# Optimization experiments

Hardware: AMD Instinct MI355X
Metric: run time of the kernel (lower is better)

## Reference

```python
import jax, jax.numpy as jnp
import numpy as np

N = 2048   # nodes in the input graph
NB = 2048  # nodes in the barycenter graph
D = 128    # embedding (feature) dimension
K = 16     # number of atoms (len(size_atoms))


def cost_mat(cost_s, cost_t, p_s, p_t, tran, emb_s, emb_t):
    """Fused Gromov-Wasserstein cost matrix.

    GW structural part:  (C_s^2 p_s) 1^T + 1 (p_t^T (C_t^2)^T) - 2 C_s T C_t^T
    Fused feature part:  0.5 * squared Euclidean distance between node embeddings.
    """
    f1 = (cost_s ** 2) @ p_s                     # (N, 1)
    f2 = p_t.T @ (cost_t ** 2).T                 # (1, NB)
    cost = f1 + f2 - 2.0 * (cost_s @ tran) @ cost_t.T  # (N, NB)
    # pairwise squared Euclidean distances between embeddings
    d_emb = (jnp.sum(emb_s ** 2, axis=1, keepdims=True)
             + jnp.sum(emb_t ** 2, axis=1)[None, :]
             - 2.0 * emb_s @ emb_t.T)            # (N, NB)
    return cost + 0.5 * d_emb


def setup_inputs() -> dict:
    key = jax.random.key(0)
    k = jax.random.split(key, 6)
    graph = jax.random.uniform(k[0], (N, N), dtype=jnp.float32)
    embedding = jax.random.normal(k[1], (N, D), dtype=jnp.float32)
    prob = jnp.ones((N, 1), jnp.float32) / N           # uniform node distribution
    graph_b = jax.random.uniform(k[2], (NB, NB), dtype=jnp.float32)
    embedding_b = jax.random.normal(k[3], (NB, D), dtype=jnp.float32)
    prob_b = jnp.ones((NB, 1), jnp.float32) / NB
    t = jax.random.uniform(k[4], (N, NB), dtype=jnp.float32)
    tran = t / jnp.sum(t)                              # valid coupling-like plan (sums to 1)
    weights = jax.nn.softmax(jax.random.normal(k[5], (K,), dtype=jnp.float32))
    return {"graph": graph, "embedding": embedding, "prob": prob,
            "graph_b": graph_b, "embedding_b": embedding_b, "prob_b": prob_b,
            "tran": tran, "weights": weights, "ole_coeff": 1, "idx": 0}


def reference(graph, embedding, prob, graph_b, embedding_b, prob_b, tran, weights, ole_coeff, idx):
    # NOTE: the torch forward also computes cluster/entropy (OLE) losses from
    # `weights`, but they do NOT enter the returned value, which is only
    # <cost_mat(...), tran>. We therefore return exactly that inner product.
    cost = cost_mat(graph, graph_b, prob, prob_b, tran, embedding, embedding_b)
    return jnp.sum(cost * tran)
```

## Files before the change

### kernel.cpp

```cpp
#include <hip/hip_runtime.h>
#include <hip/hip_bf16.h>

#define NN 2048
#define DD 128

typedef unsigned short u16;
typedef unsigned int u32;
typedef __attribute__((ext_vector_type(8))) short bf16x8;
typedef __attribute__((ext_vector_type(4))) float f32x4;

__device__ __forceinline__ u16 f2bf(float f){
  u32 u = __float_as_uint(f);
  u32 r = (u + 0x7fffu + ((u >> 16) & 1u)) >> 16;
  return (u16)r;
}

__device__ __forceinline__ void gload16(const void* g, void* l){
  __builtin_amdgcn_global_load_lds(
      (const __attribute__((address_space(1))) u32*)g,
      (__attribute__((address_space(3))) u32*)l, 16, 0, 0);
}


__device__ __forceinline__ void rowpass_graph_body(
    int bid, int tid, const float* __restrict__ src, const float* __restrict__ w,
    u16* __restrict__ dst, float* __restrict__ red){
  int wid = tid >> 6, lane = tid & 63;
  int row = bid * 4 + wid;
  const float4* s4 = (const float4*)(src + (size_t)row * NN);
  float acc = 0.f;
  #pragma unroll
  for (int it = 0; it < NN / 256; ++it){
    int c4 = it * 64 + lane;
    float4 v = s4[c4];
    float4 ww = ((const float4*)w)[c4];
    acc += v.x*v.x*ww.x + v.y*v.y*ww.y + v.z*v.z*ww.z + v.w*v.w*ww.w;
    ushort4 o; o.x = f2bf(v.x); o.y = f2bf(v.y); o.z = f2bf(v.z); o.w = f2bf(v.w);
    ((ushort4*)(dst + (size_t)row * NN))[c4] = o;
  }
  #pragma unroll
  for (int off = 32; off; off >>= 1) acc += __shfl_down(acc, off);
  if (lane == 0) red[row] = acc;
}

__device__ __forceinline__ void tran_pass_body(
    int bx, int by, int t, float (*tile)[65],
    const float* __restrict__ src,
    u16* __restrict__ Tm, u16* __restrict__ Tt,
    float* __restrict__ rs, float* __restrict__ cls)
{
  int r0 = bx * 64, c0 = by * 64;
  #pragma unroll
  for (int it = 0; it < 4; ++it){
    int chunk = it * 256 + t; int r = chunk >> 4, c4 = chunk & 15;
    float4 v = ((const float4*)(src + (size_t)(r0 + r) * NN + c0))[c4];
    tile[r][c4*4+0] = v.x; tile[r][c4*4+1] = v.y;
    tile[r][c4*4+2] = v.z; tile[r][c4*4+3] = v.w;
    ushort4 o; o.x = f2bf(v.x); o.y = f2bf(v.y); o.z = f2bf(v.z); o.w = f2bf(v.w);
    ((ushort4*)(Tm + (size_t)(r0 + r) * NN + c0))[c4] = o;
  }
  __syncthreads();
  #pragma unroll
  for (int it = 0; it < 4; ++it){
    int chunk = it * 256 + t; int j = chunk >> 4, i4 = chunk & 15;
    ushort4 o;
    o.x = f2bf(tile[i4*4+0][j]); o.y = f2bf(tile[i4*4+1][j]);
    o.z = f2bf(tile[i4*4+2][j]); o.w = f2bf(tile[i4*4+3][j]);
    ((ushort4*)(Tt + (size_t)(c0 + j) * NN + r0))[i4] = o;
  }
  {
    int r = t >> 2, cq = (t & 3) * 16;
    float s = 0.f;
    #pragma unroll
    for (int c = 0; c < 16; ++c) s += tile[r][cq + c];
    s += __shfl_down(s, 2);
    s += __shfl_down(s, 1);
    if ((t & 3) == 0) atomicAdd(&rs[r0 + r], s);
  }
  {
    int c = t >> 2, rq = (t & 3) * 16;
    float s = 0.f;
    #pragma unroll
    for (int r = 0; r < 16; ++r) s += tile[rq + r][c];
    s += __shfl_down(s, 2);
    s += __shfl_down(s, 1);
    if ((t & 3) == 0) atomicAdd(&cls[c0 + c], s);
  }
}

__device__ __forceinline__ void graphb_pass_body(
    int bx, int by, int t, float (*tile)[65], float* pb,
    const float* __restrict__ src, const float* __restrict__ probb,
    u16* __restrict__ CtT, float* __restrict__ f2)
{
  int r0 = bx * 64, c0 = by * 64;
  if (t < 64) pb[t] = probb[c0 + t];
  #pragma unroll
  for (int it = 0; it < 4; ++it){
    int chunk = it * 256 + t; int r = chunk >> 4, c4 = chunk & 15;
    float4 v = ((const float4*)(src + (size_t)(r0 + r) * NN + c0))[c4];
    tile[r][c4*4+0] = v.x; tile[r][c4*4+1] = v.y;
    tile[r][c4*4+2] = v.z; tile[r][c4*4+3] = v.w;
  }
  __syncthreads();
  #pragma unroll
  for (int it = 0; it < 4; ++it){
    int chunk = it * 256 + t; int j = chunk >> 4, i4 = chunk & 15;
    ushort4 o;
    o.x = f2bf(tile[i4*4+0][j]); o.y = f2bf(tile[i4*4+1][j]);
    o.z = f2bf(tile[i4*4+2][j]); o.w = f2bf(tile[i4*4+3][j]);
    ((ushort4*)(CtT + (size_t)(c0 + j) * NN + r0))[i4] = o;
  }
  {
    int r = t >> 2, cq = (t & 3) * 16;
    float s = 0.f;
    #pragma unroll
    for (int c = 0; c < 16; ++c){ float v = tile[r][cq + c]; s += v * v * pb[cq + c]; }
    s += __shfl_down(s, 2);
    s += __shfl_down(s, 1);
    if ((t & 3) == 0) atomicAdd(&f2[r0 + r], s);
  }
}

__device__ __forceinline__ void emb_body(
    int bid, int t, const float* __restrict__ src, u16* __restrict__ dst,
    float* __restrict__ nrm){
  int rloc = t >> 5, lane32 = t & 31;
  int row = bid * 8 + rloc;
  float4 v = ((const float4*)(src + (size_t)row * DD))[lane32];
  float a = v.x*v.x + v.y*v.y + v.z*v.z + v.w*v.w;
  ushort4 o; o.x = f2bf(v.x); o.y = f2bf(v.y); o.z = f2bf(v.z); o.w = f2bf(v.w);
  ((ushort4*)(dst + (size_t)row * DD))[lane32] = o;
  #pragma unroll
  for (int off = 16; off; off >>= 1) a += __shfl_down(a, off, 32);
  if (lane32 == 0) nrm[row] = a;
}

__global__ __launch_bounds__(256) void k_prep(
    const float* __restrict__ graph,  const float* __restrict__ prob,
    const float* __restrict__ tran,   const float* __restrict__ graphb,
    const float* __restrict__ probb,  const float* __restrict__ emb,
    const float* __restrict__ embb,
    u16* Cs, u16* Tm, u16* Tt, u16* CtT, u16* es, u16* et,
    float* f1, float* f2, float* rs, float* cls, float* ss, float* st)
{
  __shared__ float tile[64][65];
  __shared__ float pb[64];
  int b = blockIdx.x, t = threadIdx.x;
  if (b < 512){
    rowpass_graph_body(b, t, graph, prob, Cs, f1);
  } else if (b < 1536){
    int b2 = b - 512;  tran_pass_body(b2 & 31, b2 >> 5, t, tile, tran, Tm, Tt, rs, cls);
  } else if (b < 2560){
    int b2 = b - 1536; graphb_pass_body(b2 & 31, b2 >> 5, t, tile, pb, graphb, probb, CtT, f2);
  } else if (b < 2816){
    emb_body(b - 2560, t, emb, es, ss);
  } else {
    emb_body(b - 2816, t, embb, et, st);
  }
}

__global__ __launch_bounds__(512, 2) void k_gw(
    const u16* __restrict__ Cs, const u16* __restrict__ Tt,
    const u16* __restrict__ Tm, const u16* __restrict__ CtT,
    float* __restrict__ accs)
{
  __shared__ u16 lds[2][4][8192];
  const int tid = threadIdx.x;
  const int bid = blockIdx.x;
  const int swz = (bid & 7) * 32 + (bid >> 3);
  const int bi = swz >> 4, bk = swz & 15;

  const u16* srcs[4] = {Cs, Tt, Tm, CtT};
  const int panels[4] = {bi * 128, bk * 128, bi * 128, bk * 128};

  const int w = tid >> 6, lane = tid & 63;
  const int l15 = lane & 15, g = lane >> 4;
  const int gsel = w >> 2, wg = w & 3, wr = wg >> 1, wc = wg & 1;

  const int s_row = tid >> 3;
  const int s_gslot = (tid & 7) ^ (s_row & 7);

  f32x4 acc[4][4];
  #pragma unroll
  for (int m = 0; m < 4; ++m)
    #pragma unroll
    for (int n = 0; n < 4; ++n)
      acc[m][n] = (f32x4){0.f, 0.f, 0.f, 0.f};

  int offA[4][2], offB[4][2];
  #pragma unroll
  for (int m = 0; m < 4; ++m){
    int row = wr * 64 + m * 16 + l15;
    int rowb = wc * 64 + m * 16 + l15;
    #pragma unroll
    for (int kk = 0; kk < 2; ++kk){
      offA[m][kk] = row * 64 + ((((kk << 2) | g)) ^ (row & 7)) * 8;
      offB[m][kk] = rowb * 64 + ((((kk << 2) | g)) ^ (rowb & 7)) * 8;
    }
  }

  auto stage = [&](int buf, int kt){
    const size_t col = (size_t)kt * 64 + s_gslot * 8;
    #pragma unroll
    for (int tt = 0; tt < 4; ++tt){
      gload16(srcs[tt] + (size_t)(panels[tt] + s_row) * NN + col,
              &lds[buf][tt][w * 512]);
      gload16(srcs[tt] + (size_t)(panels[tt] + s_row + 64) * NN + col,
              &lds[buf][tt][4096 + w * 512]);
    }
  };

  const int NT = NN / 64;
  stage(0, 0);
  stage(1, 1);
  for (int kt = 0; kt < NT; ++kt){
    int cur = kt & 1;
    asm volatile("s_waitcnt vmcnt(8)" ::: "memory");
    __builtin_amdgcn_s_barrier();

    const u16* tA = &lds[cur][gsel * 2][0];
    const u16* tB = &lds[cur][gsel * 2 + 1][0];
    bf16x8 av[4][2], bv[4][2];
    #pragma unroll
    for (int kk = 0; kk < 2; ++kk){
      #pragma unroll
      for (int m = 0; m < 4; ++m) av[m][kk] = *(const bf16x8*)(tA + offA[m][kk]);
      #pragma unroll
      for (int n = 0; n < 4; ++n) bv[n][kk] = *(const bf16x8*)(tB + offB[n][kk]);
    }
    #pragma unroll
    for (int kk = 0; kk < 2; ++kk)
      #pragma unroll
      for (int m = 0; m < 4; ++m)
        #pragma unroll
        for (int n = 0; n < 4; ++n)
          acc[m][n] = __builtin_amdgcn_mfma_f32_16x16x32_bf16(av[m][kk], bv[n][kk], acc[m][n], 0, 0, 0);

    __builtin_amdgcn_s_barrier();

    int kn = (kt + 2 < NT) ? (kt + 2) : (NT - 1);
    stage(cur, kn);
  }

  __syncthreads();

  float* ustash = (float*)&lds[0][0][0];
  if (gsel == 0){
    #pragma unroll
    for (int m = 0; m < 4; ++m)
      #pragma unroll
      for (int n = 0; n < 4; ++n)
        #pragma unroll
        for (int r = 0; r < 4; ++r){
          int row = wr * 64 + m * 16 + g * 4 + r;
          int col = wc * 64 + n * 16 + l15;
          ustash[row * 128 + col] = acc[m][n][r];
        }
  }
  __syncthreads();
  if (gsel == 1){
    float part = 0.f;
    #pragma unroll
    for (int m = 0; m < 4; ++m)
      #pragma unroll
      for (int n = 0; n < 4; ++n)
        #pragma unroll
        for (int r = 0; r < 4; ++r){
          int row = wr * 64 + m * 16 + g * 4 + r;
          int col = wc * 64 + n * 16 + l15;
          part += acc[m][n][r] * ustash[row * 128 + col];
        }
    #pragma unroll
    for (int off = 32; off; off >>= 1) part += __shfl_down(part, off);
    if (lane == 0) atomicAdd(&accs[0], part);
  }
}

__global__ __launch_bounds__(256, 2) void k_embdot(
    const u16* __restrict__ es, const u16* __restrict__ et,
    const float* __restrict__ tran, float* __restrict__ accs)
{
  __shared__ u16 lds[2][16384];
  const int tid = threadIdx.x;
  const int bid = blockIdx.x;
  const int swz = (bid & 7) * 32 + (bid >> 3);
  const int bi = swz >> 4, bj = swz & 15;
  const int w = tid >> 6, lane = tid & 63;
  const int l15 = lane & 15, g = lane >> 4;
  const int wr = w >> 1, wc = w & 1;

  const u16* srcs[2] = {es, et};
  const int panels[2] = {bi * 128, bj * 128};

  #pragma unroll
  for (int tt = 0; tt < 2; ++tt){
    #pragma unroll
    for (int it = 0; it < 8; ++it){
      int chunk = w * 8 + it;
      int r = chunk * 4 + g;
      int s = l15 ^ (r & 15);
      gload16(srcs[tt] + (size_t)(panels[tt] + r) * DD + s * 8,
              &lds[tt][chunk * 512]);
    }
  }
  __syncthreads();

  f32x4 acc[4][4];
  #pragma unroll
  for (int m = 0; m < 4; ++m)
    #pragma unroll
    for (int n = 0; n < 4; ++n)
      acc[m][n] = (f32x4){0.f, 0.f, 0.f, 0.f};

  #pragma unroll
  for (int ks = 0; ks < 4; ++ks){
    bf16x8 av[4], bv[4];
    #pragma unroll
    for (int m = 0; m < 4; ++m){
      int row = wr * 64 + m * 16 + l15;
      int sp = (ks * 4 + g) ^ (row & 15);
      av[m] = *(const bf16x8*)((const char*)&lds[0][0] + row * 256 + sp * 16);
    }
    #pragma unroll
    for (int n = 0; n < 4; ++n){
      int rowb = wc * 64 + n * 16 + l15;
      int spb = (ks * 4 + g) ^ (rowb & 15);
      bv[n] = *(const bf16x8*)((const char*)&lds[1][0] + rowb * 256 + spb * 16);
    }
    #pragma unroll
    for (int m = 0; m < 4; ++m)
      #pragma unroll
      for (int n = 0; n < 4; ++n)
        acc[m][n] = __builtin_amdgcn_mfma_f32_16x16x32_bf16(av[m], bv[n], acc[m][n], 0, 0, 0);
  }

  float part = 0.f;
  #pragma unroll
  for (int m = 0; m < 4; ++m)
    #pragma unroll
    for (int n = 0; n < 4; ++n)
      #pragma unroll
      for (int r = 0; r < 4; ++r){
        int row = bi * 128 + wr * 64 + m * 16 + g * 4 + r;
        int col = bj * 128 + wc * 64 + n * 16 + l15;
        part += tran[(size_t)row * NN + col] * acc[m][n][r];
      }
  #pragma unroll
  for (int off = 32; off; off >>= 1) part += __shfl_down(part, off);
  if (lane == 0) atomicAdd(&accs[1], part);
}

__global__ void k_final(const float* __restrict__ f1, const float* __restrict__ f2,
                        const float* __restrict__ rowsum, const float* __restrict__ colsum,
                        const float* __restrict__ ss, const float* __restrict__ st,
                        const float* __restrict__ accs, float* out){
  __shared__ float red[256];
  int t = threadIdx.x;
  float part = 0.f;
  for (int i = t; i < NN; i += 256){
    part += (f1[i] + 0.5f * ss[i]) * rowsum[i];
    part += (f2[i] + 0.5f * st[i]) * colsum[i];
  }
  red[t] = part; __syncthreads();
  for (int s = 128; s; s >>= 1){ if (t < s) red[t] += red[t + s]; __syncthreads(); }
  if (t == 0){
    float total = red[0] - 2.0f * accs[0] - accs[1];
    out[0] = total;
  }
}

extern "C" void kernel_launch(void* const* d_in, const int* in_sizes, int n_in,
                              void* d_out, int out_size, void* d_ws, size_t ws_size,
                              hipStream_t stream)
{
  const float* graph  = (const float*)d_in[0];
  const float* emb    = (const float*)d_in[1];
  const float* prob   = (const float*)d_in[2];
  const float* graphb = (const float*)d_in[3];
  const float* embb   = (const float*)d_in[4];
  const float* probb  = (const float*)d_in[5];
  const float* tran   = (const float*)d_in[6];
  (void)in_sizes; (void)n_in; (void)out_size; (void)ws_size;

  char* ws = (char*)d_ws;
  u16* Cs   = (u16*)(ws + 0);
  u16* Tm   = (u16*)(ws + 8388608);
  u16* Tt   = (u16*)(ws + 16777216);
  u16* CtT  = (u16*)(ws + 25165824);
  u16* es   = (u16*)(ws + 33554432);
  u16* et   = (u16*)(ws + 34078720);
  float* f1   = (float*)(ws + 34603008);
  float* f2   = (float*)(ws + 34611200);
  float* rs   = (float*)(ws + 34619392);
  float* cls  = (float*)(ws + 34627584);
  float* ss   = (float*)(ws + 34635776);
  float* st   = (float*)(ws + 34643968);
  float* accs = (float*)(ws + 34652160);

  hipMemsetAsync(ws + 34603008, 0, 49216, stream);

  k_prep<<<3072, 256, 0, stream>>>(graph, prob, tran, graphb, probb, emb, embb,
                                   Cs, Tm, Tt, CtT, es, et,
                                   f1, f2, rs, cls, ss, st);
  k_gw<<<256, 512, 0, stream>>>(Cs, Tt, Tm, CtT, accs);
  k_embdot<<<256, 256, 0, stream>>>(es, et, tran, accs);
  k_final<<<1, 256, 0, stream>>>(f1, f2, rs, cls, ss, st, accs, (float*)d_out);
}
```

Baseline: 95.15 us.

## Fuse GW, embedding-dot and final reduction into one kernel with last-block finish

Merges the GW MFMA kernel, the embedding dot kernel and the final scalar reduction into a single 512-block launch. Blocks 0-255 do the GW product and blocks 256-511 do the embedding product with 8 waves. A global atomic counter elects the last block to run the final reduction. The GW loop is also reordered to issue the next stage's loads before the MFMAs, with an explicit lgkmcnt wait and a sched barrier. This removes two launches and lets the small embedding work overlap the GW tiles, at the cost of relying on the counter being zeroed by the memset and on correct fencing.

```diff
diff --git a/kernel.cpp b/kernel.cpp
--- a/kernel.cpp
+++ b/kernel.cpp
@@ -160,213 +160,217 @@
   }
 }
 
-__global__ __launch_bounds__(512, 2) void k_gw(
+__global__ __launch_bounds__(512, 2) void k_main(
     const u16* __restrict__ Cs, const u16* __restrict__ Tt,
     const u16* __restrict__ Tm, const u16* __restrict__ CtT,
-    float* __restrict__ accs)
+    const u16* __restrict__ es, const u16* __restrict__ et,
+    const float* __restrict__ tran,
+    const float* __restrict__ f1, const float* __restrict__ f2,
+    const float* __restrict__ rs, const float* __restrict__ cls,
+    const float* __restrict__ ss, const float* __restrict__ st,
+    float* __restrict__ accs, u32* __restrict__ ctr, float* __restrict__ out)
 {
   __shared__ u16 lds[2][4][8192];
+  __shared__ unsigned flagS;
   const int tid = threadIdx.x;
   const int bid = blockIdx.x;
-  const int swz = (bid & 7) * 32 + (bid >> 3);
-  const int bi = swz >> 4, bk = swz & 15;
-
-  const u16* srcs[4] = {Cs, Tt, Tm, CtT};
-  const int panels[4] = {bi * 128, bk * 128, bi * 128, bk * 128};
-
   const int w = tid >> 6, lane = tid & 63;
   const int l15 = lane & 15, g = lane >> 4;
-  const int gsel = w >> 2, wg = w & 3, wr = wg >> 1, wc = wg & 1;
-
-  const int s_row = tid >> 3;
-  const int s_gslot = (tid & 7) ^ (s_row & 7);
-
-  f32x4 acc[4][4];
-  #pragma unroll
-  for (int m = 0; m < 4; ++m)
-    #pragma unroll
-    for (int n = 0; n < 4; ++n)
-      acc[m][n] = (f32x4){0.f, 0.f, 0.f, 0.f};
-
-  int offA[4][2], offB[4][2];
-  #pragma unroll
-  for (int m = 0; m < 4; ++m){
-    int row = wr * 64 + m * 16 + l15;
-    int rowb = wc * 64 + m * 16 + l15;
-    #pragma unroll
-    for (int kk = 0; kk < 2; ++kk){
-      offA[m][kk] = row * 64 + ((((kk << 2) | g)) ^ (row & 7)) * 8;
-      offB[m][kk] = rowb * 64 + ((((kk << 2) | g)) ^ (rowb & 7)) * 8;
-    }
-  }
-
-  auto stage = [&](int buf, int kt){
-    const size_t col = (size_t)kt * 64 + s_gslot * 8;
-    #pragma unroll
-    for (int tt = 0; tt < 4; ++tt){
-      gload16(srcs[tt] + (size_t)(panels[tt] + s_row) * NN + col,
-              &lds[buf][tt][w * 512]);
-      gload16(srcs[tt] + (size_t)(panels[tt] + s_row + 64) * NN + col,
-              &lds[buf][tt][4096 + w * 512]);
-    }
-  };
-
-  const int NT = NN / 64;
-  stage(0, 0);
-  stage(1, 1);
-  for (int kt = 0; kt < NT; ++kt){
-    int cur = kt & 1;
-    asm volatile("s_waitcnt vmcnt(8)" ::: "memory");
-    __builtin_amdgcn_s_barrier();
-
-    const u16* tA = &lds[cur][gsel * 2][0];
-    const u16* tB = &lds[cur][gsel * 2 + 1][0];
-    bf16x8 av[4][2], bv[4][2];
-    #pragma unroll
-    for (int kk = 0; kk < 2; ++kk){
-      #pragma unroll
-      for (int m = 0; m < 4; ++m) av[m][kk] = *(const bf16x8*)(tA + offA[m][kk]);
-      #pragma unroll
-      for (int n = 0; n < 4; ++n) bv[n][kk] = *(const bf16x8*)(tB + offB[n][kk]);
-    }
-    #pragma unroll
-    for (int kk = 0; kk < 2; ++kk)
-      #pragma unroll
-      for (int m = 0; m < 4; ++m)
-        #pragma unroll
-        for (int n = 0; n < 4; ++n)
-          acc[m][n] = __builtin_amdgcn_mfma_f32_16x16x32_bf16(av[m][kk], bv[n][kk], acc[m][n], 0, 0, 0);
-
-    __builtin_amdgcn_s_barrier();
-
-    int kn = (kt + 2 < NT) ? (kt + 2) : (NT - 1);
-    stage(cur, kn);
-  }
-
-  __syncthreads();
-
-  float* ustash = (float*)&lds[0][0][0];
-  if (gsel == 0){
+
+  if (bid < 256){
+    const int swz = (bid & 7) * 32 + (bid >> 3);
+    const int bi = swz >> 4, bk = swz & 15;
+    const u16* srcs[4] = {Cs, Tt, Tm, CtT};
+    const int panels[4] = {bi * 128, bk * 128, bi * 128, bk * 128};
+    const int gsel = w >> 2, wg = w & 3, wr = wg >> 1, wc = wg & 1;
+    const int s_row = tid >> 3;
+    const int s_gslot = (tid & 7) ^ (s_row & 7);
+
+    f32x4 acc[4][4];
     #pragma unroll
     for (int m = 0; m < 4; ++m)
       #pragma unroll
       for (int n = 0; n < 4; ++n)
-        #pragma unroll
-        for (int r = 0; r < 4; ++r){
-          int row = wr * 64 + m * 16 + g * 4 + r;
-          int col = wc * 64 + n * 16 + l15;
-          ustash[row * 128 + col] = acc[m][n][r];
-        }
-  }
-  __syncthreads();
-  if (gsel == 1){
-    float part = 0.f;
-    #pragma unroll
-    for (int m = 0; m < 4; ++m)
-      #pragma unroll
-      for (int n = 0; n < 4; ++n)
-        #pragma unroll
-        for (int r = 0; r < 4; ++r){
-          int row = wr * 64 + m * 16 + g * 4 + r;
-          int col = wc * 64 + n * 16 + l15;
-          part += acc[m][n][r] * ustash[row * 128 + col];
-        }
-    #pragma unroll
-    for (int off = 32; off; off >>= 1) part += __shfl_down(part, off);
-    if (lane == 0) atomicAdd(&accs[0], part);
-  }
-}
-
-__global__ __launch_bounds__(256, 2) void k_embdot(
-    const u16* __restrict__ es, const u16* __restrict__ et,
-    const float* __restrict__ tran, float* __restrict__ accs)
-{
-  __shared__ u16 lds[2][16384];
-  const int tid = threadIdx.x;
-  const int bid = blockIdx.x;
-  const int swz = (bid & 7) * 32 + (bid >> 3);
-  const int bi = swz >> 4, bj = swz & 15;
-  const int w = tid >> 6, lane = tid & 63;
-  const int l15 = lane & 15, g = lane >> 4;
-  const int wr = w >> 1, wc = w & 1;
-
-  const u16* srcs[2] = {es, et};
-  const int panels[2] = {bi * 128, bj * 128};
-
-  #pragma unroll
-  for (int tt = 0; tt < 2; ++tt){
-    #pragma unroll
-    for (int it = 0; it < 8; ++it){
-      int chunk = w * 8 + it;
-      int r = chunk * 4 + g;
-      int s = l15 ^ (r & 15);
-      gload16(srcs[tt] + (size_t)(panels[tt] + r) * DD + s * 8,
-              &lds[tt][chunk * 512]);
-    }
-  }
-  __syncthreads();
-
-  f32x4 acc[4][4];
-  #pragma unroll
-  for (int m = 0; m < 4; ++m)
-    #pragma unroll
-    for (int n = 0; n < 4; ++n)
-      acc[m][n] = (f32x4){0.f, 0.f, 0.f, 0.f};
-
-  #pragma unroll
-  for (int ks = 0; ks < 4; ++ks){
-    bf16x8 av[4], bv[4];
+        acc[m][n] = (f32x4){0.f, 0.f, 0.f, 0.f};
+
+    int offA[4][2], offB[4][2];
     #pragma unroll
     for (int m = 0; m < 4; ++m){
       int row = wr * 64 + m * 16 + l15;
-      int sp = (ks * 4 + g) ^ (row & 15);
-      av[m] = *(const bf16x8*)((const char*)&lds[0][0] + row * 256 + sp * 16);
-    }
-    #pragma unroll
-    for (int n = 0; n < 4; ++n){
-      int rowb = wc * 64 + n * 16 + l15;
-      int spb = (ks * 4 + g) ^ (rowb & 15);
-      bv[n] = *(const bf16x8*)((const char*)&lds[1][0] + rowb * 256 + spb * 16);
-    }
+      int rowb = wc * 64 + m * 16 + l15;
+      #pragma unroll
+      for (int kk = 0; kk < 2; ++kk){
+        offA[m][kk] = row * 64 + ((((kk << 2) | g)) ^ (row & 7)) * 8;
+        offB[m][kk] = rowb * 64 + ((((kk << 2) | g)) ^ (rowb & 7)) * 8;
+      }
+    }
+
+    auto stage = [&](int buf, int kt){
+      const size_t col = (size_t)kt * 64 + s_gslot * 8;
+      #pragma unroll
+      for (int tt = 0; tt < 4; ++tt){
+        gload16(srcs[tt] + (size_t)(panels[tt] + s_row) * NN + col,
+                &lds[buf][tt][w * 512]);
+        gload16(srcs[tt] + (size_t)(panels[tt] + s_row + 64) * NN + col,
+                &lds[buf][tt][4096 + w * 512]);
+      }
+    };
+
+    const int NT = NN / 64;
+    stage(0, 0);
+    stage(1, 1);
+    for (int kt = 0; kt < NT; ++kt){
+      int cur = kt & 1;
+      asm volatile("s_waitcnt vmcnt(8)" ::: "memory");
+      __builtin_amdgcn_s_barrier();
+
+      const u16* tA = &lds[cur][gsel * 2][0];
+      const u16* tB = &lds[cur][gsel * 2 + 1][0];
+      bf16x8 av[4][2], bv[4][2];
+      #pragma unroll
+      for (int kk = 0; kk < 2; ++kk){
+        #pragma unroll
+        for (int m = 0; m < 4; ++m) av[m][kk] = *(const bf16x8*)(tA + offA[m][kk]);
+        #pragma unroll
+        for (int n = 0; n < 4; ++n) bv[n][kk] = *(const bf16x8*)(tB + offB[n][kk]);
+      }
+      asm volatile("s_waitcnt lgkmcnt(0)" ::: "memory");
+      __builtin_amdgcn_sched_barrier(0);
+      __builtin_amdgcn_s_barrier();
+
+      int kn = (kt + 2 < NT) ? (kt + 2) : (NT - 1);
+      stage(cur, kn);
+
+      #pragma unroll
+      for (int kk = 0; kk < 2; ++kk)
+        #pragma unroll
+        for (int m = 0; m < 4; ++m)
+          #pragma unroll
+          for (int n = 0; n < 4; ++n)
+            acc[m][n] = __builtin_amdgcn_mfma_f32_16x16x32_bf16(av[m][kk], bv[n][kk], acc[m][n], 0, 0, 0);
+    }
+
+    __syncthreads();
+
+    float* ustash = (float*)&lds[0][0][0];
+    if (gsel == 0){
+      #pragma unroll
+      for (int m = 0; m < 4; ++m)
+        #pragma unroll
+        for (int n = 0; n < 4; ++n)
+          #pragma unroll
+          for (int r = 0; r < 4; ++r){
+            int row = wr * 64 + m * 16 + g * 4 + r;
+            int col = wc * 64 + n * 16 + l15;
+            ustash[row * 128 + col] = acc[m][n][r];
+          }
+    }
+    __syncthreads();
+    if (gsel == 1){
+      float part = 0.f;
+      #pragma unroll
+      for (int m = 0; m < 4; ++m)
+        #pragma unroll
+        for (int n = 0; n < 4; ++n)
+          #pragma unroll
+          for (int r = 0; r < 4; ++r){
+            int row = wr * 64 + m * 16 + g * 4 + r;
+            int col = wc * 64 + n * 16 + l15;
+            part += acc[m][n][r] * ustash[row * 128 + col];
+          }
+      #pragma unroll
+      for (int off = 32; off; off >>= 1) part += __shfl_down(part, off);
+      if (lane == 0) atomicAdd(&accs[0], part);
+    }
+  } else {
+    const int eid = bid - 256;
+    const int swz = (eid & 7) * 32 + (eid >> 3);
+    const int bi = swz >> 4, bj = swz & 15;
+    const int wr = w >> 2, wc = w & 3;
+    u16* elds = &lds[0][0][0];
+
+    const u16* srcs[2] = {es, et};
+    const int panels[2] = {bi * 128, bj * 128};
+
+    #pragma unroll
+    for (int tt = 0; tt < 2; ++tt){
+      #pragma unroll
+      for (int it = 0; it < 4; ++it){
+        int chunk = w * 4 + it;
+        int r = chunk * 4 + g;
+        int s = l15 ^ (r & 15);
+        gload16(srcs[tt] + (size_t)(panels[tt] + r) * DD + s * 8,
+                &elds[tt * 16384 + chunk * 512]);
+      }
+    }
+    __syncthreads();
+
+    f32x4 acc[4][2];
     #pragma unroll
     for (int m = 0; m < 4; ++m)
       #pragma unroll
-      for (int n = 0; n < 4; ++n)
-        acc[m][n] = __builtin_amdgcn_mfma_f32_16x16x32_bf16(av[m], bv[n], acc[m][n], 0, 0, 0);
-  }
-
-  float part = 0.f;
-  #pragma unroll
-  for (int m = 0; m < 4; ++m)
-    #pragma unroll
-    for (int n = 0; n < 4; ++n)
-      #pragma unroll
-      for (int r = 0; r < 4; ++r){
-        int row = bi * 128 + wr * 64 + m * 16 + g * 4 + r;
-        int col = bj * 128 + wc * 64 + n * 16 + l15;
-        part += tran[(size_t)row * NN + col] * acc[m][n][r];
-      }
-  #pragma unroll
-  for (int off = 32; off; off >>= 1) part += __shfl_down(part, off);
-  if (lane == 0) atomicAdd(&accs[1], part);
-}
-
-__global__ void k_final(const float* __restrict__ f1, const float* __restrict__ f2,
-                        const float* __restrict__ rowsum, const float* __restrict__ colsum,
-                        const float* __restrict__ ss, const float* __restrict__ st,
-                        const float* __restrict__ accs, float* out){
-  __shared__ float red[256];
-  int t = threadIdx.x;
-  float part = 0.f;
-  for (int i = t; i < NN; i += 256){
-    part += (f1[i] + 0.5f * ss[i]) * rowsum[i];
-    part += (f2[i] + 0.5f * st[i]) * colsum[i];
-  }
-  red[t] = part; __syncthreads();
-  for (int s = 128; s; s >>= 1){ if (t < s) red[t] += red[t + s]; __syncthreads(); }
-  if (t == 0){
-    float total = red[0] - 2.0f * accs[0] - accs[1];
-    out[0] = total;
+      for (int n = 0; n < 2; ++n)
+        acc[m][n] = (f32x4){0.f, 0.f, 0.f, 0.f};
+
+    #pragma unroll
+    for (int ks = 0; ks < 4; ++ks){
+      bf16x8 av[4], bv[2];
+      #pragma unroll
+      for (int m = 0; m < 4; ++m){
+        int row = wr * 64 + m * 16 + l15;
+        int sp = (ks * 4 + g) ^ (row & 15);
+        av[m] = *(const bf16x8*)(elds + row * 128 + sp * 8);
+      }
+      #pragma unroll
+      for (int n = 0; n < 2; ++n){
+        int rowb = wc * 32 + n * 16 + l15;
+        int spb = (ks * 4 + g) ^ (rowb & 15);
+        bv[n] = *(const bf16x8*)(elds + 16384 + rowb * 128 + spb * 8);
+      }
+      #pragma unroll
+      for (int m = 0; m < 4; ++m)
+        #pragma unroll
+        for (int n = 0; n < 2; ++n)
+          acc[m][n] = __builtin_amdgcn_mfma_f32_16x16x32_bf16(av[m], bv[n], acc[m][n], 0, 0, 0);
+    }
+
+    float part = 0.f;
+    #pragma unroll
+    for (int m = 0; m < 4; ++m)
+      #pragma unroll
+      for (int n = 0; n < 2; ++n)
+        #pragma unroll
+        for (int r = 0; r < 4; ++r){
+          int row = bi * 128 + wr * 64 + m * 16 + g * 4 + r;
+          int col = bj * 128 + wc * 32 + n * 16 + l15;
+          part += tran[(size_t)row * NN + col] * acc[m][n][r];
+        }
+    #pragma unroll
+    for (int off = 32; off; off >>= 1) part += __shfl_down(part, off);
+    if (lane == 0) atomicAdd(&accs[1], part);
+  }
+
+  __syncthreads();
+  if (tid == 0){
+    __threadfence();
+    unsigned d = atomicAdd(ctr, 1u);
+    flagS = (d == 511u) ? 1u : 0u;
+  }
+  __syncthreads();
+  if (flagS){
+    __threadfence();
+    float* red = (float*)&lds[0][0][0];
+    float part = 0.f;
+    for (int i = tid; i < NN; i += 512){
+      part += (f1[i] + 0.5f * ss[i]) * rs[i];
+      part += (f2[i] + 0.5f * st[i]) * cls[i];
+    }
+    red[tid] = part; __syncthreads();
+    for (int s = 256; s; s >>= 1){
+      if (tid < s) red[tid] += red[tid + s];
+      __syncthreads();
+    }
+    if (tid == 0) out[0] = red[0] - 2.0f * accs[0] - accs[1];
   }
 }
 
@@ -397,13 +401,14 @@
   float* ss   = (float*)(ws + 34635776);
   float* st   = (float*)(ws + 34643968);
   float* accs = (float*)(ws + 34652160);
+  u32*   ctr  = (u32*)(ws + 34652192);
 
   hipMemsetAsync(ws + 34603008, 0, 49216, stream);
 
   k_prep<<<3072, 256, 0, stream>>>(graph, prob, tran, graphb, probb, emb, embb,
                                    Cs, Tm, Tt, CtT, es, et,
                                    f1, f2, rs, cls, ss, st);
-  k_gw<<<256, 512, 0, stream>>>(Cs, Tt, Tm, CtT, accs);
-  k_embdot<<<256, 256, 0, stream>>>(es, et, tran, accs);
-  k_final<<<1, 256, 0, stream>>>(f1, f2, rs, cls, ss, st, accs, (float*)d_out);
-}
+  k_main<<<512, 512, 0, stream>>>(Cs, Tt, Tm, CtT, es, et, tran,
+                                  f1, f2, rs, cls, ss, st,
+                                  accs, ctr, (float*)d_out);
+}
```

Result: slower. 111.8 us (+17.5%).
